# Performance work log

Hardware: AMD Instinct MI355X
Metric: run time of the kernel (lower is better)

Reference implementation:

```python
import jax, jax.numpy as jnp
import numpy as np

NEG_SLOPE = 0.2
MASK_FILL = -1e9

N, F_IN, K, F_OUT = 4096, 512, 8, 128


def setup_inputs() -> dict:
    key = jax.random.key(0)
    k1, k2, k3, k4, k5 = jax.random.split(key, 5)
    x = jax.random.normal(k1, (N, F_IN), dtype=jnp.float32)
    mask = jax.random.randint(k2, (N, N), 0, 2).astype(jnp.bool_)
    # ensure no fully-masked row (self loops)
    mask = mask | jnp.eye(N, dtype=jnp.bool_)
    # xavier-ish scaled params
    W = jax.random.normal(k3, (K * F_OUT, F_IN), dtype=jnp.float32) * (2.0 / (F_IN + K * F_OUT)) ** 0.5
    b = jnp.zeros((K * F_OUT,), dtype=jnp.float32)
    a_left = jax.random.normal(k4, (K, F_OUT), dtype=jnp.float32) * (2.0 / (1 + F_OUT)) ** 0.5
    a_right = jax.random.normal(k5, (K, F_OUT), dtype=jnp.float32) * (2.0 / (1 + F_OUT)) ** 0.5
    return {"x": x, "mask": mask, "W": W, "b": b, "a_left": a_left, "a_right": a_right}


def reference(x, mask, W, b, a_left, a_right):
    # Linear projection: (N, K*F') -> (N, K, F')
    h = (x @ W.T + b).reshape(x.shape[0], K, F_OUT)
    # Additive attention logits: e[k,n,m] = leaky_relu(a_left.h_n + a_right.h_m)
    left = jnp.einsum('nkf,kf->kn', h, a_left)    # (K, N)
    right = jnp.einsum('mkf,kf->km', h, a_right)  # (K, N)
    e = jax.nn.leaky_relu(left[:, :, None] + right[:, None, :], NEG_SLOPE)  # (K,N,N)
    # Mask out non-neighbors, softmax over neighbor axis m
    e = jnp.where(mask[None, :, :], e, MASK_FILL)
    a = jax.nn.softmax(e, axis=-1)  # (K, N, N)
    # Weighted aggregation (eq. 4) + ELU
    h_prime = jax.nn.elu(jnp.einsum('knm,mkf->nkf', a, h))  # (N, K, F')
    # Concat heads (eq. 5): (N, K*F')
    return h_prime.reshape(h_prime.shape[0], -1)
```

## Files before the change

kernel.cpp:

```cpp
#include <hip/hip_runtime.h>
#include <hip/hip_bf16.h>

typedef unsigned short u16;
typedef __attribute__((ext_vector_type(8))) short short8;
typedef __attribute__((ext_vector_type(2))) float f32x2;
typedef __attribute__((ext_vector_type(4))) float f32x4;
typedef __attribute__((ext_vector_type(16))) float f32x16;

#define N_NODES 4096
#define FIN 512
#define KH 8
#define FO 128
#define DM 1024
#define LOG2E 1.44269504088896340736f

__device__ __forceinline__ void gload16(const u16* g, u16* l) {
    __builtin_amdgcn_global_load_lds(
        (const __attribute__((address_space(1))) unsigned int*)g,
        (__attribute__((address_space(3))) unsigned int*)l,
        16, 0, 0);
}

__device__ __forceinline__ unsigned pk_bf16(float lo, float hi) {
    unsigned r;
    asm("v_cvt_pk_bf16_f32 %0, %1, %2" : "=v"(r) : "v"(lo), "v"(hi));
    return r;
}

__global__ __launch_bounds__(256) void split_bf16(const float* __restrict__ src,
                                                  u16* __restrict__ hi,
                                                  u16* __restrict__ lo,
                                                  int n4) {
    int idx = blockIdx.x * 256 + threadIdx.x;
    if (idx >= n4) return;
    float4 v = ((const float4*)src)[idx];
    unsigned h01 = pk_bf16(v.x, v.y);
    unsigned h23 = pk_bf16(v.z, v.w);
    float hx = __uint_as_float(h01 << 16);
    float hy = __uint_as_float(h01 & 0xffff0000u);
    float hz = __uint_as_float(h23 << 16);
    float hw = __uint_as_float(h23 & 0xffff0000u);
    unsigned l01 = pk_bf16(v.x - hx, v.y - hy);
    unsigned l23 = pk_bf16(v.z - hz, v.w - hw);
    uint2 hv; hv.x = h01; hv.y = h23;
    uint2 lv; lv.x = l01; lv.y = l23;
    ((uint2*)hi)[idx] = hv;
    ((uint2*)lo)[idx] = lv;
}

__global__ __launch_bounds__(512) void gemm_mfma(const u16* __restrict__ Xh,
                                                 const u16* __restrict__ Xl,
                                                 const u16* __restrict__ Wh,
                                                 const u16* __restrict__ Wl,
                                                 const float* __restrict__ bias,
                                                 const float* __restrict__ aL,
                                                 const float* __restrict__ aR,
                                                 float2* __restrict__ C2,
                                                 unsigned* __restrict__ D2b,
                                                 u16* __restrict__ HbT) {
    const int khead = blockIdx.x;
    const int n0 = blockIdx.y * 128;
    const int tid = threadIdx.x;
    const int w = tid >> 6, lane = tid & 63;
    const int wr = w >> 1, wc = w & 1;
    const int c = lane & 31, half = lane >> 5;

    __shared__ u16 S[2][16384];

    const int sa = w >> 1;
    const int shv = w & 1;
    const int scl = lane & 3;
    const int ssw = ((lane >> 2) ^ (lane >> 4)) & 3;
    const int sgc = scl ^ ssw;
    const u16* gb; int growbase;
    if (sa == 0)      { gb = Xh; growbase = n0; }
    else if (sa == 1) { gb = Xl; growbase = n0; }
    else if (sa == 2) { gb = Wh; growbase = khead * 128; }
    else              { gb = Wl; growbase = khead * 128; }
    const u16* glb = gb + (size_t)(growbase + shv * 64 + (lane >> 2)) * FIN + sgc * 8;
    const int sldsoff = sa * 4096 + shv * 64 * 32;

    const int sw = ((c) ^ (c >> 2)) & 3;
    const int aoff = (wr * 32 + c) * 32;
    const int boff0 = 8192 + (wc * 64 + c) * 32;
    const int boff1 = 8192 + (wc * 64 + 32 + c) * 32;

    f32x16 acc0, acc1;
#pragma unroll
    for (int i = 0; i < 16; ++i) { acc0[i] = 0.f; acc1[i] = 0.f; }

#pragma unroll
    for (int i = 0; i < 4; ++i)
        gload16(glb + (size_t)i * 16 * FIN, &S[0][sldsoff + i * 512]);
    __syncthreads();

    int cur = 0;
    for (int kt = 0; kt < 16; ++kt) {
        if (kt < 15) {
            const u16* gsrc = glb + (kt + 1) * 32;
            u16* dst = &S[cur ^ 1][sldsoff];
#pragma unroll
            for (int i = 0; i < 4; ++i)
                gload16(gsrc + (size_t)i * 16 * FIN, dst + i * 512);
        }

        const u16* sp = S[cur];
        short8 ah[2], al8[2], bh[2][2], bl8[2][2];
#pragma unroll
        for (int ks = 0; ks < 2; ++ks) {
            int ch = ((ks * 2 + half) ^ sw) * 8;
            ah[ks]     = *(const short8*)&sp[aoff + ch];
            al8[ks]    = *(const short8*)&sp[4096 + aoff + ch];
            bh[0][ks]  = *(const short8*)&sp[boff0 + ch];
            bl8[0][ks] = *(const short8*)&sp[boff0 + 4096 + ch];
            bh[1][ks]  = *(const short8*)&sp[boff1 + ch];
            bl8[1][ks] = *(const short8*)&sp[boff1 + 4096 + ch];
        }
#pragma unroll
        for (int ks = 0; ks < 2; ++ks) {
            acc0 = __builtin_amdgcn_mfma_f32_32x32x16_bf16(ah[ks], bh[0][ks], acc0, 0, 0, 0);
            acc0 = __builtin_amdgcn_mfma_f32_32x32x16_bf16(ah[ks], bl8[0][ks], acc0, 0, 0, 0);
            acc0 = __builtin_amdgcn_mfma_f32_32x32x16_bf16(al8[ks], bh[0][ks], acc0, 0, 0, 0);
            acc1 = __builtin_amdgcn_mfma_f32_32x32x16_bf16(ah[ks], bh[1][ks], acc1, 0, 0, 0);
            acc1 = __builtin_amdgcn_mfma_f32_32x32x16_bf16(ah[ks], bl8[1][ks], acc1, 0, 0, 0);
            acc1 = __builtin_amdgcn_mfma_f32_32x32x16_bf16(al8[ks], bh[1][ks], acc1, 0, 0, 0);
        }
        __syncthreads();
        cur ^= 1;
    }

    const int fglob = khead * FO + wc * 64 + c;
    float b0 = bias[fglob], b1 = bias[fglob + 32];
#pragma unroll
    for (int r = 0; r < 16; ++r) { acc0[r] += b0; acc1[r] += b1; }

    float alv0 = aL[fglob], alv1 = aL[fglob + 32];
    float arv0 = aR[fglob], arv1 = aR[fglob + 32];
    float pl[16], pr[16];
#pragma unroll
    for (int r = 0; r < 16; ++r) {
        pl[r] = acc0[r] * alv0 + acc1[r] * alv1;
        pr[r] = acc0[r] * arv0 + acc1[r] * arv1;
    }
#pragma unroll
    for (int off = 1; off < 32; off <<= 1) {
#pragma unroll
        for (int r = 0; r < 16; ++r) {
            pl[r] += __shfl_xor(pl[r], off);
            pr[r] += __shfl_xor(pr[r], off);
        }
    }

    u16* T = &S[0][0];
    float* LRf = (float*)&S[0][0] + 9216;

    if (c == 0) {
#pragma unroll
        for (int r = 0; r < 16; ++r) {
            int node = wr * 32 + (r & 3) + 8 * (r >> 2) + 4 * half;
            LRf[(wc * 2 + 0) * 128 + node] = pl[r];
            LRf[(wc * 2 + 1) * 128 + node] = pr[r];
        }
    }

#pragma unroll
    for (int q = 0; q < 4; ++q) {
        int nb = wr * 32 + q * 8 + 4 * half;
        unsigned p00 = pk_bf16(acc0[q * 4 + 0], acc0[q * 4 + 1]);
        unsigned p01 = pk_bf16(acc0[q * 4 + 2], acc0[q * 4 + 3]);
        unsigned p10 = pk_bf16(acc1[q * 4 + 0], acc1[q * 4 + 1]);
        unsigned p11 = pk_bf16(acc1[q * 4 + 2], acc1[q * 4 + 3]);
        *(unsigned*)&T[(wc * 64 + c) * 136 + nb]      = p00;
        *(unsigned*)&T[(wc * 64 + c) * 136 + nb + 2]  = p01;
        *(unsigned*)&T[(wc * 64 + 32 + c) * 136 + nb]     = p10;
        *(unsigned*)&T[(wc * 64 + 32 + c) * 136 + nb + 2] = p11;
    }
    __syncthreads();

    if (wc == 0) {
        int node = wr * 32 + (lane & 31);
        if (lane < 32) {
            float L = (LRf[0 * 128 + node] + LRf[2 * 128 + node]) * LOG2E;
            float2 cv; cv.x = exp2f(L); cv.y = exp2f(0.2f * L);
            C2[(size_t)khead * N_NODES + n0 + node] = cv;
        } else {
            float R = (LRf[1 * 128 + node] + LRf[3 * 128 + node]) * LOG2E;
            D2b[(size_t)khead * N_NODES + n0 + node] = pk_bf16(exp2f(R), exp2f(0.2f * R));
        }
    }

    {
        int f = tid >> 2, q = tid & 3;
        const uint4* src = (const uint4*)&T[f * 136 + q * 32];
        uint4* dst = (uint4*)(HbT + (size_t)(khead * FO + f) * N_NODES + n0 + q * 32);
#pragma unroll
        for (int u = 0; u < 4; ++u) dst[u] = src[u];
    }
}

__global__ __launch_bounds__(256) void pack_mask(const int* __restrict__ mask,
                                                 unsigned long long* __restrict__ mb) {
    int gid = blockIdx.x * 256 + threadIdx.x;
    int wid = gid >> 6, lane = gid & 63;
    int v = mask[(size_t)wid * 64 + lane];
    unsigned long long bits = __ballot(v != 0);
    if (lane == 0) mb[wid] = bits;
}

__global__ __launch_bounds__(512, 4) void gat_attn(const u16* __restrict__ HbT,
                                                   const float2* __restrict__ C2,
                                                   const unsigned* __restrict__ D2b,
                                                   const unsigned* __restrict__ mb32,
                                                   float* __restrict__ out) {
    const int blk = blockIdx.x;
    const int k = blk & 7;
    const int n0 = (blk >> 3) * 64;
    const int tid = threadIdx.x;
    const int w = tid >> 6, lane = tid & 63;
    const int ns = w & 1, g = (w >> 1) & 1, ks = w >> 2;
    const int fr = lane & 15, kg = lane >> 4;

    __shared__ u16 Ht[2][2][128 * 64];

    const int na0 = n0 + ns * 32 + fr;
    const int na1 = na0 + 16;
    const float2 c0f = C2[(size_t)k * N_NODES + na0];
    const float2 c1f = C2[(size_t)k * N_NODES + na1];
    const float cx0 = c0f.x, cy0 = c0f.y;
    const float cx1 = c1f.x, cy1 = c1f.y;
    const unsigned* mp0 = mb32 + (size_t)na0 * 128 + g * 64 + ks;
    const unsigned* mp1 = mb32 + (size_t)na1 * 128 + g * 64 + ks;

    f32x4 acc[2][9];
#pragma unroll
    for (int s = 0; s < 2; ++s)
#pragma unroll
        for (int c = 0; c < 9; ++c) acc[s][c] = 0.f;

    const short o1 = (fr == 0) ? (short)0x3F80 : (short)0;
    const short8 ones = {o1, o1, o1, o1, o1, o1, o1, o1};

    const int q = ns * 2 + ks;
    const int fsub = lane >> 3;
    const int seg = ((lane & 7) ^ fsub) * 8;
    const u16* gstage = HbT + (size_t)(k * FO + q * 32 + fsub) * N_NODES + g * 2048 + seg;
    u16* lbA = &Ht[g][0][q * 2048];
    u16* lbB = &Ht[g][1][q * 2048];

    const int frx = fr & 7;
    const int offb = fr * 64 + ((ks * 4 + kg) ^ frx) * 8;

    const unsigned* D2k = D2b + (size_t)k * N_NODES + g * 2048 + ks * 32 + kg * 8;

#pragma unroll
    for (int j = 0; j < 4; ++j)
        gload16(gstage + (size_t)j * 8 * N_NODES, lbA + j * 512);
    asm volatile("s_waitcnt vmcnt(0)" ::: "memory");
    __builtin_amdgcn_s_barrier();

#define ATTN_STEP(RBUF, SBUF, MT) do {                                                  \
    const int mtv = (MT);                                                               \
               \
    const unsigned* dp = D2k + mtv * 64;                                                \
    uint4 d0 = *(const uint4*)(dp);                                                     \
    uint4 d1 = *(const uint4*)(dp + 4);                                                 \
    unsigned m0w = mp0[mtv * 2];                                                        \
    unsigned m1w = mp1[mtv * 2];                                                        \
                                                                    \
    if (mtv < 31) {                                                                     \
        const u16* gs = gstage + ((size_t)(mtv + 1) << 6);                              \
        _Pragma("unroll")                                                               \
        for (int j = 0; j < 4; ++j)                                                     \
            gload16(gs + (size_t)j * 8 * N_NODES, (SBUF) + j * 512);                    \
    }                                                                                   \
    __builtin_amdgcn_sched_barrier(0);                                                  \
                                            \
    {                                                                                   \
        unsigned mq0 = m0w >> (kg * 8);                                                 \
        unsigned mq1 = m1w >> (kg * 8);                                                 \
        unsigned wa[8] = {d0.x, d0.y, d0.z, d0.w, d1.x, d1.y, d1.z, d1.w};              \
        union { unsigned u[4]; short8 s; } ua, ub;                                      \
        _Pragma("unroll")                                                               \
        for (int vp = 0; vp < 4; ++vp) {                                                \
            unsigned u0 = wa[2 * vp], u1 = wa[2 * vp + 1];                              \
            float dx0 = __uint_as_float(u0 << 16);                                      \
            float dy0 = __uint_as_float(u0 & 0xffff0000u);                              \
            float dx1 = __uint_as_float(u1 << 16);                                      \
            float dy1 = __uint_as_float(u1 & 0xffff0000u);                              \
            unsigned s00 = (unsigned)(((int)(mq0 << (31 - 2 * vp))) >> 31);             \
            unsigned s01 = (unsigned)(((int)(mq0 << (30 - 2 * vp))) >> 31);             \
            unsigned s10 = (unsigned)(((int)(mq1 << (31 - 2 * vp))) >> 31);             \
            unsigned s11 = (unsigned)(((int)(mq1 << (30 - 2 * vp))) >> 31);             \
            float q0a = __uint_as_float(__float_as_uint(fmaxf(cx0 * dx0, cy0 * dy0)) & s00); \
            float q0b = __uint_as_float(__float_as_uint(fmaxf(cx0 * dx1, cy0 * dy1)) & s01); \
            float q1a = __uint_as_float(__float_as_uint(fmaxf(cx1 * dx0, cy1 * dy0)) & s10); \
            float q1b = __uint_as_float(__float_as_uint(fmaxf(cx1 * dx1, cy1 * dy1)) & s11); \
            ua.u[vp] = pk_bf16(q0a, q0b);                                               \
            ub.u[vp] = pk_bf16(q1a, q1b);                                               \
        }                                                                               \
        short8 a0 = ua.s, a1 = ub.s;                                                    \
                            \
        const u16* hb = (RBUF);                                                         \
        __builtin_amdgcn_s_setprio(1);                                                  \
        _Pragma("unroll")                                                               \
        for (int c = 0; c < 8; ++c) {                                                   \
            short8 b = *(const short8*)(hb + c * 1024 + offb);                          \
            acc[0][c] = __builtin_amdgcn_mfma_f32_16x16x32_bf16(a0, b, acc[0][c], 0, 0, 0); \
            acc[1][c] = __builtin_amdgcn_mfma_f32_16x16x32_bf16(a1, b, acc[1][c], 0, 0, 0); \
        }                                                                               \
        acc[0][8] = __builtin_amdgcn_mfma_f32_16x16x32_bf16(a0, ones, acc[0][8], 0, 0, 0);  \
        acc[1][8] = __builtin_amdgcn_mfma_f32_16x16x32_bf16(a1, ones, acc[1][8], 0, 0, 0);  \
        __builtin_amdgcn_s_setprio(0);                                                  \
    }                                                                                   \
                        \
    asm volatile("s_waitcnt lgkmcnt(0)" ::: "memory");                                  \
    asm volatile("s_waitcnt vmcnt(0)" ::: "memory");                                    \
    __builtin_amdgcn_s_barrier();                                                       \
} while (0)

    {
        const u16* rb0 = &Ht[g][0][0];
        const u16* rb1 = &Ht[g][1][0];
        for (int mt = 0; mt < 32; mt += 2) {
            ATTN_STEP(rb0, lbB, mt);
            ATTN_STEP(rb1, lbA, mt + 1);
        }
    }
#undef ATTN_STEP

    __syncthreads();

    float* fb = (float*)&Ht[0][0][0];
    const int myid = g + 2 * ks;
    const int cb = ns * 4608 + lane;
    for (int src = 1; src < 4; ++src) {
        if (myid == src) {
#pragma unroll
            for (int s = 0; s < 2; ++s)
#pragma unroll
                for (int c = 0; c < 9; ++c)
#pragma unroll
                    for (int j = 0; j < 4; ++j)
                        fb[cb + (((s * 9 + c) * 4 + j) << 6)] = acc[s][c][j];
        }
        __syncthreads();
        if (myid == 0) {
#pragma unroll
            for (int s = 0; s < 2; ++s)
#pragma unroll
                for (int c = 0; c < 9; ++c)
#pragma unroll
                    for (int j = 0; j < 4; ++j)
                        acc[s][c][j] += fb[cb + (((s * 9 + c) * 4 + j) << 6)];
        }
        __syncthreads();
    }

    if (myid == 0) {
#pragma unroll
        for (int s = 0; s < 2; ++s) {
#pragma unroll
            for (int j = 0; j < 4; ++j) {
                float S = __shfl(acc[s][8][j], (lane & 48));
                float inv = 1.0f / S;
                int n_out = n0 + ns * 32 + s * 16 + kg * 4 + j;
                float* orow = out + (size_t)n_out * DM + k * FO + fr;
#pragma unroll
                for (int c = 0; c < 8; ++c) {
                    float v = acc[s][c][j] * inv;
                    float e = v > 0.f ? v : (__expf(v) - 1.0f);
                    orow[c * 16] = e;
                }
            }
        }
    }
}

extern "C" void kernel_launch(void* const* d_in, const int* in_sizes, int n_in,
                              void* d_out, int out_size, void* d_ws, size_t ws_size,
                              hipStream_t stream) {
    const float* x = (const float*)d_in[0];
    const int* mask = (const int*)d_in[1];
    const float* W = (const float*)d_in[2];
    const float* bias = (const float*)d_in[3];
    const float* aL = (const float*)d_in[4];
    const float* aR = (const float*)d_in[5];
    float* out = (float*)d_out;

    char* ws = (char*)d_ws;
    u16* Xh = (u16*)ws;   ws += (size_t)N_NODES * FIN * 2;
    u16* Xl = (u16*)ws;   ws += (size_t)N_NODES * FIN * 2;
    u16* Wh = (u16*)ws;   ws += (size_t)DM * FIN * 2;
    u16* Wl = (u16*)ws;   ws += (size_t)DM * FIN * 2;
    u16* HbT = (u16*)ws;  ws += (size_t)KH * FO * N_NODES * 2;
    float2* C2 = (float2*)ws;  ws += (size_t)KH * N_NODES * 8;
    unsigned* D2b = (unsigned*)ws; ws += (size_t)KH * N_NODES * 4;
    unsigned long long* mb = (unsigned long long*)ws;

    split_bf16<<<dim3(2048), dim3(256), 0, stream>>>(x, Xh, Xl, N_NODES * FIN / 4);
    split_bf16<<<dim3(512), dim3(256), 0, stream>>>(W, Wh, Wl, DM * FIN / 4);
    gemm_mfma<<<dim3(8, 32), dim3(512), 0, stream>>>(Xh, Xl, Wh, Wl, bias, aL, aR,
                                                     C2, D2b, HbT);
    pack_mask<<<dim3(65536), dim3(256), 0, stream>>>(mask, mb);
    gat_attn<<<dim3(512), dim3(512), 0, stream>>>(HbT, C2, D2b, (const unsigned*)mb, out);
}
```

Baseline: 125.7 us.

## Load attention B-operand directly from global instead of LDS double buffering

The attention kernel drops the LDS staging of HbT tiles (global_load_lds double buffer with a barrier per step). Each wave now reads its B fragments straight from global/L2 and owns a contiguous quarter of the neighbor axis, processing 64 columns per iteration with two MFMAs per accumulator. This removes the per-step barriers and LDS traffic and frees most of the shared memory. In exchange it relies on cache hits for redundant global reads of H across waves, with strided 16-byte loads and no explicit prefetch.

```diff
diff --git a/kernel.cpp b/kernel.cpp
--- a/kernel.cpp
+++ b/kernel.cpp
@@ -207,20 +207,39 @@
     if (lane == 0) mb[wid] = bits;
 }
 
+__device__ __forceinline__ short8 pgen8(float cx, float cy, uint4 w0, uint4 w1,
+                                        unsigned m32) {
+    unsigned wa[8] = {w0.x, w0.y, w0.z, w0.w, w1.x, w1.y, w1.z, w1.w};
+    union { unsigned u[4]; short8 s; } r;
+#pragma unroll
+    for (int vp = 0; vp < 4; ++vp) {
+        unsigned u0 = wa[2 * vp], u1 = wa[2 * vp + 1];
+        float pa = fmaxf(cx * __uint_as_float(u0 << 16),
+                         cy * __uint_as_float(u0 & 0xffff0000u));
+        float pb = fmaxf(cx * __uint_as_float(u1 << 16),
+                         cy * __uint_as_float(u1 & 0xffff0000u));
+        unsigned sa = (unsigned)(((int)(m32 << (31 - 2 * vp))) >> 31);
+        unsigned sb = (unsigned)(((int)(m32 << (30 - 2 * vp))) >> 31);
+        r.u[vp] = pk_bf16(__uint_as_float(__float_as_uint(pa) & sa),
+                          __uint_as_float(__float_as_uint(pb) & sb));
+    }
+    return r.s;
+}
+
 __global__ __launch_bounds__(512, 4) void gat_attn(const u16* __restrict__ HbT,
                                                    const float2* __restrict__ C2,
                                                    const unsigned* __restrict__ D2b,
-                                                   const unsigned* __restrict__ mb32,
+                                                   const unsigned long long* __restrict__ mb,
                                                    float* __restrict__ out) {
     const int blk = blockIdx.x;
     const int k = blk & 7;
     const int n0 = (blk >> 3) * 64;
     const int tid = threadIdx.x;
     const int w = tid >> 6, lane = tid & 63;
-    const int ns = w & 1, g = (w >> 1) & 1, ks = w >> 2;
+    const int ns = w & 1, mq = w >> 1;
     const int fr = lane & 15, kg = lane >> 4;
 
-    __shared__ u16 Ht[2][2][128 * 64];
+    __shared__ float fb[9216];
 
     const int na0 = n0 + ns * 32 + fr;
     const int na1 = na0 + 16;
@@ -228,8 +247,8 @@
     const float2 c1f = C2[(size_t)k * N_NODES + na1];
     const float cx0 = c0f.x, cy0 = c0f.y;
     const float cx1 = c1f.x, cy1 = c1f.y;
-    const unsigned* mp0 = mb32 + (size_t)na0 * 128 + g * 64 + ks;
-    const unsigned* mp1 = mb32 + (size_t)na1 * 128 + g * 64 + ks;
+    const unsigned long long* mrow0 = mb + (size_t)na0 * 64 + mq * 16;
+    const unsigned long long* mrow1 = mb + (size_t)na1 * 64 + mq * 16;
 
     f32x4 acc[2][9];
 #pragma unroll
@@ -240,101 +259,44 @@
     const short o1 = (fr == 0) ? (short)0x3F80 : (short)0;
     const short8 ones = {o1, o1, o1, o1, o1, o1, o1, o1};
 
-    const int q = ns * 2 + ks;
-    const int fsub = lane >> 3;
-    const int seg = ((lane & 7) ^ fsub) * 8;
-    const u16* gstage = HbT + (size_t)(k * FO + q * 32 + fsub) * N_NODES + g * 2048 + seg;
-    u16* lbA = &Ht[g][0][q * 2048];
-    u16* lbB = &Ht[g][1][q * 2048];
-
-    const int frx = fr & 7;
-    const int offb = fr * 64 + ((ks * 4 + kg) ^ frx) * 8;
-
-    const unsigned* D2k = D2b + (size_t)k * N_NODES + g * 2048 + ks * 32 + kg * 8;
-
-#pragma unroll
-    for (int j = 0; j < 4; ++j)
-        gload16(gstage + (size_t)j * 8 * N_NODES, lbA + j * 512);
-    asm volatile("s_waitcnt vmcnt(0)" ::: "memory");
-    __builtin_amdgcn_s_barrier();
-
-#define ATTN_STEP(RBUF, SBUF, MT) do {                                                  \
-    const int mtv = (MT);                                                               \
-               \
-    const unsigned* dp = D2k + mtv * 64;                                                \
-    uint4 d0 = *(const uint4*)(dp);                                                     \
-    uint4 d1 = *(const uint4*)(dp + 4);                                                 \
-    unsigned m0w = mp0[mtv * 2];                                                        \
-    unsigned m1w = mp1[mtv * 2];                                                        \
-                                                                    \
-    if (mtv < 31) {                                                                     \
-        const u16* gs = gstage + ((size_t)(mtv + 1) << 6);                              \
-        _Pragma("unroll")                                                               \
-        for (int j = 0; j < 4; ++j)                                                     \
-            gload16(gs + (size_t)j * 8 * N_NODES, (SBUF) + j * 512);                    \
-    }                                                                                   \
-    __builtin_amdgcn_sched_barrier(0);                                                  \
-                                            \
-    {                                                                                   \
-        unsigned mq0 = m0w >> (kg * 8);                                                 \
-        unsigned mq1 = m1w >> (kg * 8);                                                 \
-        unsigned wa[8] = {d0.x, d0.y, d0.z, d0.w, d1.x, d1.y, d1.z, d1.w};              \
-        union { unsigned u[4]; short8 s; } ua, ub;                                      \
-        _Pragma("unroll")                                                               \
-        for (int vp = 0; vp < 4; ++vp) {                                                \
-            unsigned u0 = wa[2 * vp], u1 = wa[2 * vp + 1];                              \
-            float dx0 = __uint_as_float(u0 << 16);                                      \
-            float dy0 = __uint_as_float(u0 & 0xffff0000u);                              \
-            float dx1 = __uint_as_float(u1 << 16);                                      \
-            float dy1 = __uint_as_float(u1 & 0xffff0000u);                              \
-            unsigned s00 = (unsigned)(((int)(mq0 << (31 - 2 * vp))) >> 31);             \
-            unsigned s01 = (unsigned)(((int)(mq0 << (30 - 2 * vp))) >> 31);             \
-            unsigned s10 = (unsigned)(((int)(mq1 << (31 - 2 * vp))) >> 31);             \
-            unsigned s11 = (unsigned)(((int)(mq1 << (30 - 2 * vp))) >> 31);             \
-            float q0a = __uint_as_float(__float_as_uint(fmaxf(cx0 * dx0, cy0 * dy0)) & s00); \
-            float q0b = __uint_as_float(__float_as_uint(fmaxf(cx0 * dx1, cy0 * dy1)) & s01); \
-            float q1a = __uint_as_float(__float_as_uint(fmaxf(cx1 * dx0, cy1 * dy0)) & s10); \
-            float q1b = __uint_as_float(__float_as_uint(fmaxf(cx1 * dx1, cy1 * dy1)) & s11); \
-            ua.u[vp] = pk_bf16(q0a, q0b);                                               \
-            ub.u[vp] = pk_bf16(q1a, q1b);                                               \
-        }                                                                               \
-        short8 a0 = ua.s, a1 = ub.s;                                                    \
-                            \
-        const u16* hb = (RBUF);                                                         \
-        __builtin_amdgcn_s_setprio(1);                                                  \
-        _Pragma("unroll")                                                               \
-        for (int c = 0; c < 8; ++c) {                                                   \
-            short8 b = *(const short8*)(hb + c * 1024 + offb);                          \
-            acc[0][c] = __builtin_amdgcn_mfma_f32_16x16x32_bf16(a0, b, acc[0][c], 0, 0, 0); \
-            acc[1][c] = __builtin_amdgcn_mfma_f32_16x16x32_bf16(a1, b, acc[1][c], 0, 0, 0); \
-        }                                                                               \
-        acc[0][8] = __builtin_amdgcn_mfma_f32_16x16x32_bf16(a0, ones, acc[0][8], 0, 0, 0);  \
-        acc[1][8] = __builtin_amdgcn_mfma_f32_16x16x32_bf16(a1, ones, acc[1][8], 0, 0, 0);  \
-        __builtin_amdgcn_s_setprio(0);                                                  \
-    }                                                                                   \
-                        \
-    asm volatile("s_waitcnt lgkmcnt(0)" ::: "memory");                                  \
-    asm volatile("s_waitcnt vmcnt(0)" ::: "memory");                                    \
-    __builtin_amdgcn_s_barrier();                                                       \
-} while (0)
-
-    {
-        const u16* rb0 = &Ht[g][0][0];
-        const u16* rb1 = &Ht[g][1][0];
-        for (int mt = 0; mt < 32; mt += 2) {
-            ATTN_STEP(rb0, lbB, mt);
-            ATTN_STEP(rb1, lbA, mt + 1);
-        }
-    }
-#undef ATTN_STEP
-
-    __syncthreads();
-
-    float* fb = (float*)&Ht[0][0][0];
-    const int myid = g + 2 * ks;
+    const u16* bbase = HbT + (size_t)(k * FO + fr) * N_NODES + mq * 1024 + kg * 8;
+    const unsigned* D2k = D2b + (size_t)k * N_NODES + mq * 1024 + kg * 8;
+    const int shA = kg * 8, shB = shA + 32;
+
+    for (int t = 0; t < 16; ++t) {
+        const int m0 = t * 64;
+        const unsigned* dp = D2k + m0;
+        uint4 dA0 = *(const uint4*)(dp);
+        uint4 dA1 = *(const uint4*)(dp + 4);
+        uint4 dB0 = *(const uint4*)(dp + 32);
+        uint4 dB1 = *(const uint4*)(dp + 36);
+        unsigned long long bits0 = mrow0[t];
+        unsigned long long bits1 = mrow1[t];
+
+        short8 aA0 = pgen8(cx0, cy0, dA0, dA1, (unsigned)(bits0 >> shA));
+        short8 aB0 = pgen8(cx0, cy0, dB0, dB1, (unsigned)(bits0 >> shB));
+        short8 aA1 = pgen8(cx1, cy1, dA0, dA1, (unsigned)(bits1 >> shA));
+        short8 aB1 = pgen8(cx1, cy1, dB0, dB1, (unsigned)(bits1 >> shB));
+
+        const u16* bp = bbase + m0;
+#pragma unroll
+        for (int c = 0; c < 8; ++c) {
+            short8 bA = *(const short8*)(bp + (size_t)c * 16 * N_NODES);
+            short8 bB = *(const short8*)(bp + (size_t)c * 16 * N_NODES + 32);
+            acc[0][c] = __builtin_amdgcn_mfma_f32_16x16x32_bf16(aA0, bA, acc[0][c], 0, 0, 0);
+            acc[0][c] = __builtin_amdgcn_mfma_f32_16x16x32_bf16(aB0, bB, acc[0][c], 0, 0, 0);
+            acc[1][c] = __builtin_amdgcn_mfma_f32_16x16x32_bf16(aA1, bA, acc[1][c], 0, 0, 0);
+            acc[1][c] = __builtin_amdgcn_mfma_f32_16x16x32_bf16(aB1, bB, acc[1][c], 0, 0, 0);
+        }
+        acc[0][8] = __builtin_amdgcn_mfma_f32_16x16x32_bf16(aA0, ones, acc[0][8], 0, 0, 0);
+        acc[0][8] = __builtin_amdgcn_mfma_f32_16x16x32_bf16(aB0, ones, acc[0][8], 0, 0, 0);
+        acc[1][8] = __builtin_amdgcn_mfma_f32_16x16x32_bf16(aA1, ones, acc[1][8], 0, 0, 0);
+        acc[1][8] = __builtin_amdgcn_mfma_f32_16x16x32_bf16(aB1, ones, acc[1][8], 0, 0, 0);
+    }
+
     const int cb = ns * 4608 + lane;
     for (int src = 1; src < 4; ++src) {
-        if (myid == src) {
+        if (mq == src) {
 #pragma unroll
             for (int s = 0; s < 2; ++s)
 #pragma unroll
@@ -344,7 +306,7 @@
                         fb[cb + (((s * 9 + c) * 4 + j) << 6)] = acc[s][c][j];
         }
         __syncthreads();
-        if (myid == 0) {
+        if (mq == 0) {
 #pragma unroll
             for (int s = 0; s < 2; ++s)
 #pragma unroll
@@ -356,7 +318,7 @@
         __syncthreads();
     }
 
-    if (myid == 0) {
+    if (mq == 0) {
 #pragma unroll
         for (int s = 0; s < 2; ++s) {
 #pragma unroll
@@ -402,5 +364,5 @@
     gemm_mfma<<<dim3(8, 32), dim3(512), 0, stream>>>(Xh, Xl, Wh, Wl, bias, aL, aR,
                                                      C2, D2b, HbT);
     pack_mask<<<dim3(65536), dim3(256), 0, stream>>>(mask, mb);
-    gat_attn<<<dim3(512), dim3(512), 0, stream>>>(HbT, C2, D2b, (const unsigned*)mb, out);
-}
+    gat_attn<<<dim3(512), dim3(512), 0, stream>>>(HbT, C2, D2b, mb, out);
+}
```

After: 224.5 us. 78.6% more time.
